# Optimization experiments

Hardware: AMD Instinct MI355X
Metric: run time of the kernel (lower is better)

Reference implementation:

```python
import jax, jax.numpy as jnp
import numpy as np

N, F, T, B, E, G = 50000, 3, 32, 32, 100000, 64
R = 1.1

def setup_inputs() -> dict:
    key = jax.random.key(0)
    k1, k2, k3, k4 = jax.random.split(key, 4)
    x = jax.random.normal(k1, (N, F), dtype=jnp.float32)
    v = jax.random.uniform(k2, (F, T), dtype=jnp.float32) - 0.5  # torch.rand(...) - 0.5
    lin = jnp.linspace(-R, R, B, dtype=jnp.float32).reshape(B, 1, 1)
    edge_index = jax.random.randint(k3, (2, E), 0, N)
    batch = jnp.sort(jax.random.randint(k4, (N,), 0, G))  # sorted graph ids per node
    return {"x": x, "v": v, "lin": lin, "edge_index": edge_index,
            "batch": batch, "num_graphs": G}


def _compute_ecc(h, index, lin, dim_size):
    # h: (M, T) heights; lin: (B,1,1); broadcast sigmoid -> (B, M, T)
    ecc = jax.nn.sigmoid(200.0 * (lin - h))
    # segment-sum over the M axis per graph; torch's segment_coo(...).movedim(0,1)
    # yields (dim_size, B, T), which equals segment_sum over axis 0 of (M, B, T).
    return jax.ops.segment_sum(jnp.moveaxis(ecc, 1, 0), index, num_segments=dim_size)


def reference(x, v, lin, edge_index, batch, num_graphs):
    nh = x @ v                                   # (N, T) node heights
    eh = jnp.max(nh[edge_index], axis=0)         # (E, T) edge max-gather
    ect_nodes = _compute_ecc(nh, batch, lin, num_graphs)                     # (G, B, T)
    ect_edges = _compute_ecc(eh, batch[edge_index[0]], lin, num_graphs)      # (G, B, T)
    return ect_nodes - ect_edges
```

## Files before the change

### kernel.cpp

```cpp
#include <hip/hip_runtime.h>

#define WG 256
#define G64 64
#define SPLITS 16

__global__ __launch_bounds__(WG) void k_bucket(const int* __restrict__ edge,
                                               const int* __restrict__ batch,
                                               int2* __restrict__ bucket,
                                               int* __restrict__ cursor,
                                               int* __restrict__ node_off,
                                               float* __restrict__ out,
                                               int E, int N, int CAP) {
    __shared__ int lc[G64], lb[G64];
    int tid = threadIdx.x;
    int bid = blockIdx.x;
    if (tid < G64) lc[tid] = 0;

    if (bid < G64) {
        float4* o4 = (float4*)(out + ((size_t)bid << 10));
        o4[tid] = make_float4(0.f, 0.f, 0.f, 0.f);
    }
    __syncthreads();

    int e = bid * WG + tid;
    int g = 0, r = 0, s = 0, d = 0;
    if (e < E) {
        s = edge[e];
        d = edge[E + e];
        g = batch[s];
        r = atomicAdd(&lc[g], 1);
    }
    __syncthreads();
    if (tid < G64 && lc[tid]) lb[tid] = atomicAdd(&cursor[tid], lc[tid]);
    __syncthreads();
    if (e < E) {
        int pos = lb[g] + r;
        if (pos < CAP) bucket[(size_t)g * CAP + pos] = make_int2(s, d);
    }

    if (bid == 0 && tid <= G64) {
        int lo = 0, hi = N;
        while (lo < hi) {
            int mid = (lo + hi) >> 1;
            if (batch[mid] < tid) lo = mid + 1; else hi = mid;
        }
        node_off[tid] = lo;
    }
}

__global__ __launch_bounds__(WG) void k_acc(const float* __restrict__ x,
                                            const float* __restrict__ v,
                                            const int2* __restrict__ bucket,
                                            const float* __restrict__ lin,
                                            const int* __restrict__ cursor,
                                            const int* __restrict__ node_off,
                                            float* __restrict__ out, int CAP) {
    int g = blockIdx.x;
    int n0 = node_off[g], n1 = node_off[g + 1];
    int nn = n1 - n0;
    int ne = cursor[g]; if (ne > CAP) ne = CAP;
    int L = nn + ne;
    int ipc = (L + SPLITS - 1) / SPLITS;
    int lo = blockIdx.y * ipc;
    int hi = lo + ipc; if (hi > L) hi = L;

    int tid = threadIdx.x, t = tid & 31, sub = tid >> 5;
    float v0 = v[t], v1 = v[32 + t], v2 = v[64 + t];

    float lin0 = lin[0];
    float dlin = lin[1] - lin[0];
    const float LOG2E = 1.4426950408889634f;
    float d2 = 200.f * dlin * LOG2E;
    float inv_dlin = 1.f / dlin;
    float fstep = exp2f(-d2);

    float acc[32];
#pragma unroll
    for (int b = 0; b < 32; ++b) acc[b] = 0.f;

    int nhi = hi < nn ? hi : nn;
    for (int idx = lo + sub; idx < nhi; idx += 8) {
        const float* xr = x + (size_t)(n0 + idx) * 3;
        float h = xr[0] * v0 + xr[1] * v1 + xr[2] * v2;
        float bs = (h - lin0) * inv_dlin;
        float bF = floorf(bs);
        float e0 = exp2f((bs - bF) * d2);
        float s0 = __builtin_amdgcn_rcpf(1.f + e0);
        float s1 = __builtin_amdgcn_rcpf(fmaf(e0, fstep, 1.f));
        float m = s1 - s0;
        float base = fmaf(-bF, m, s0);
#pragma unroll
        for (int b = 0; b < 32; ++b)
            acc[b] += __builtin_amdgcn_fmed3f(fmaf(m, (float)b, base), 0.f, 1.f);
    }

    int elo = lo > nn ? lo : nn;
    for (int idx = elo + sub; idx < hi; idx += 8) {
        int2 sd = bucket[(size_t)g * CAP + (idx - nn)];
        const float* xs = x + (size_t)sd.x * 3;
        const float* xd = x + (size_t)sd.y * 3;
        float hs = xs[0] * v0 + xs[1] * v1 + xs[2] * v2;
        float hd = xd[0] * v0 + xd[1] * v1 + xd[2] * v2;
        float h = fmaxf(hs, hd);
        float bs = (h - lin0) * inv_dlin;
        float bF = floorf(bs);
        float e0 = exp2f((bs - bF) * d2);
        float s0 = __builtin_amdgcn_rcpf(1.f + e0);
        float s1 = __builtin_amdgcn_rcpf(fmaf(e0, fstep, 1.f));
        float m = -(s1 - s0);
        float base = fmaf(-bF, m, -s0);
#pragma unroll
        for (int b = 0; b < 32; ++b)
            acc[b] += __builtin_amdgcn_fmed3f(fmaf(m, (float)b, base), -1.f, 0.f);
    }

    __shared__ float stage[4 * 1024];
#pragma unroll
    for (int b = 0; b < 32; ++b) acc[b] += __shfl_xor(acc[b], 32, 64);
    int w = tid >> 6;
    if ((tid & 32) == 0) {
#pragma unroll
        for (int b = 0; b < 32; ++b) stage[(w << 10) + (b << 5) + t] = acc[b];
    }
    __syncthreads();
    for (int c = tid; c < 1024; c += WG) {
        float s = stage[c] + stage[1024 + c] + stage[2048 + c] + stage[3072 + c];
        unsafeAtomicAdd(&out[((size_t)g << 10) + c], s);
    }
}

extern "C" void kernel_launch(void* const* d_in, const int* in_sizes, int n_in,
                              void* d_out, int out_size, void* d_ws, size_t ws_size,
                              hipStream_t stream) {
    const float* x     = (const float*)d_in[0];
    const float* v     = (const float*)d_in[1];
    const float* lin   = (const float*)d_in[2];
    const int*   edge  = (const int*)d_in[3];
    const int*   batch = (const int*)d_in[4];
    int N = in_sizes[4];
    int E = in_sizes[3] / 2;

    float* out = (float*)d_out;

    int* cursor   = (int*)d_ws;
    int* node_off = cursor + G64;
    int2* bucket  = (int2*)((char*)d_ws + 1024);
    long long cap_ws = (long long)((ws_size - 1024) / ((size_t)G64 * sizeof(int2)));
    int CAP = (int)(cap_ws < (long long)E ? cap_ws : (long long)E);

    hipMemsetAsync(cursor, 0, G64 * sizeof(int), stream);

    k_bucket<<<(E + WG - 1) / WG, WG, 0, stream>>>(edge, batch, bucket, cursor,
                                                   node_off, out, E, N, CAP);
    dim3 grid(G64, SPLITS);
    k_acc<<<grid, WG, 0, stream>>>(x, v, bucket, lin, cursor, node_off, out, CAP);
}
```

Baseline: 94.95 us.

## Fuse edge bucketing into accumulation kernel with per-block filtered edge scan

```diff
diff --git a/kernel.cpp b/kernel.cpp
--- a/kernel.cpp
+++ b/kernel.cpp
@@ -3,70 +3,49 @@
 #define WG 256
 #define G64 64
 #define SPLITS 16
+#define TILE 1024
 
-__global__ __launch_bounds__(WG) void k_bucket(const int* __restrict__ edge,
-                                               const int* __restrict__ batch,
-                                               int2* __restrict__ bucket,
-                                               int* __restrict__ cursor,
-                                               int* __restrict__ node_off,
-                                               float* __restrict__ out,
-                                               int E, int N, int CAP) {
-    __shared__ int lc[G64], lb[G64];
-    int tid = threadIdx.x;
-    int bid = blockIdx.x;
-    if (tid < G64) lc[tid] = 0;
 
-    if (bid < G64) {
-        float4* o4 = (float4*)(out + ((size_t)bid << 10));
-        o4[tid] = make_float4(0.f, 0.f, 0.f, 0.f);
-    }
+__device__ __forceinline__ int lbound_par(const int* __restrict__ batch, int N,
+                                          int val, int tid, int* scratch) {
+    const int stride = (N + WG - 1) / WG;
+    if (tid == 0) *scratch = N;
     __syncthreads();
-
-    int e = bid * WG + tid;
-    int g = 0, r = 0, s = 0, d = 0;
-    if (e < E) {
-        s = edge[e];
-        d = edge[E + e];
-        g = batch[s];
-        r = atomicAdd(&lc[g], 1);
-    }
+    int i0 = tid * stride;
+    if (i0 < N && batch[i0] >= val) atomicMin(scratch, i0);
     __syncthreads();
-    if (tid < G64 && lc[tid]) lb[tid] = atomicAdd(&cursor[tid], lc[tid]);
+    int hi = *scratch;
     __syncthreads();
-    if (e < E) {
-        int pos = lb[g] + r;
-        if (pos < CAP) bucket[(size_t)g * CAP + pos] = make_int2(s, d);
-    }
-
-    if (bid == 0 && tid <= G64) {
-        int lo = 0, hi = N;
-        while (lo < hi) {
-            int mid = (lo + hi) >> 1;
-            if (batch[mid] < tid) lo = mid + 1; else hi = mid;
-        }
-        node_off[tid] = lo;
-    }
+    if (tid == 0) *scratch = hi;
+    __syncthreads();
+    int lo = hi - stride + 1; if (lo < 0) lo = 0;
+    int j = lo + tid;
+    if (j < hi && batch[j] >= val) atomicMin(scratch, j);
+    __syncthreads();
+    int r = *scratch;
+    __syncthreads();
+    return r;
 }
 
-__global__ __launch_bounds__(WG) void k_acc(const float* __restrict__ x,
-                                            const float* __restrict__ v,
-                                            const int2* __restrict__ bucket,
-                                            const float* __restrict__ lin,
-                                            const int* __restrict__ cursor,
-                                            const int* __restrict__ node_off,
-                                            float* __restrict__ out, int CAP) {
-    int g = blockIdx.x;
-    int n0 = node_off[g], n1 = node_off[g + 1];
-    int nn = n1 - n0;
-    int ne = cursor[g]; if (ne > CAP) ne = CAP;
-    int L = nn + ne;
-    int ipc = (L + SPLITS - 1) / SPLITS;
-    int lo = blockIdx.y * ipc;
-    int hi = lo + ipc; if (hi > L) hi = L;
+__global__ __launch_bounds__(WG) void k_fused(const float* __restrict__ x,
+                                              const float* __restrict__ v,
+                                              const float* __restrict__ lin,
+                                              const int* __restrict__ edge,
+                                              const int* __restrict__ batch,
+                                              float* __restrict__ out,
+                                              int E, int N) {
+    __shared__ int2  queue[TILE];
+    __shared__ float stage[4 * 1024];
+    __shared__ int   qn, scratch;
 
+    int g = blockIdx.x, split = blockIdx.y;
     int tid = threadIdx.x, t = tid & 31, sub = tid >> 5;
+
+    int n0 = lbound_par(batch, N, g,     tid, &scratch);
+    int n1 = lbound_par(batch, N, g + 1, tid, &scratch);
+    if (tid == 0) qn = 0;
+
     float v0 = v[t], v1 = v[32 + t], v2 = v[64 + t];
-
     float lin0 = lin[0];
     float dlin = lin[1] - lin[0];
     const float LOG2E = 1.4426950408889634f;
@@ -78,9 +57,11 @@
 #pragma unroll
     for (int b = 0; b < 32; ++b) acc[b] = 0.f;
 
-    int nhi = hi < nn ? hi : nn;
-    for (int idx = lo + sub; idx < nhi; idx += 8) {
-        const float* xr = x + (size_t)(n0 + idx) * 3;
+    int nn = n1 - n0;
+    int a0 = n0 + (int)((long long)nn * split / SPLITS);
+    int a1 = n0 + (int)((long long)nn * (split + 1) / SPLITS);
+    for (int idx = a0 + sub; idx < a1; idx += 8) {
+        const float* xr = x + (size_t)idx * 3;
         float h = xr[0] * v0 + xr[1] * v1 + xr[2] * v2;
         float bs = (h - lin0) * inv_dlin;
         float bF = floorf(bs);
@@ -94,27 +75,43 @@
             acc[b] += __builtin_amdgcn_fmed3f(fmaf(m, (float)b, base), 0.f, 1.f);
     }
 
-    int elo = lo > nn ? lo : nn;
-    for (int idx = elo + sub; idx < hi; idx += 8) {
-        int2 sd = bucket[(size_t)g * CAP + (idx - nn)];
-        const float* xs = x + (size_t)sd.x * 3;
-        const float* xd = x + (size_t)sd.y * 3;
-        float hs = xs[0] * v0 + xs[1] * v1 + xs[2] * v2;
-        float hd = xd[0] * v0 + xd[1] * v1 + xd[2] * v2;
-        float h = fmaxf(hs, hd);
-        float bs = (h - lin0) * inv_dlin;
-        float bF = floorf(bs);
-        float e0 = exp2f((bs - bF) * d2);
-        float s0 = __builtin_amdgcn_rcpf(1.f + e0);
-        float s1 = __builtin_amdgcn_rcpf(fmaf(e0, fstep, 1.f));
-        float m = -(s1 - s0);
-        float base = fmaf(-bF, m, -s0);
+    int c0 = (int)((long long)E * split / SPLITS);
+    int c1 = (int)((long long)E * (split + 1) / SPLITS);
+    __syncthreads();
+    for (int ts = c0; ts < c1; ts += TILE) {
+        int te = ts + TILE; if (te > c1) te = c1;
+        for (int i = ts + tid; i < te; i += WG) {
+            int s = edge[i];
+            if (s >= n0 && s < n1) {
+                int k = atomicAdd(&qn, 1);
+                queue[k] = make_int2(s, edge[E + i]);
+            }
+        }
+        __syncthreads();
+        int q = qn;
+        for (int k = sub; k < q; k += 8) {
+            int2 sd = queue[k];
+            const float* xs = x + (size_t)sd.x * 3;
+            const float* xd = x + (size_t)sd.y * 3;
+            float hs = xs[0] * v0 + xs[1] * v1 + xs[2] * v2;
+            float hd = xd[0] * v0 + xd[1] * v1 + xd[2] * v2;
+            float h = fmaxf(hs, hd);
+            float bs = (h - lin0) * inv_dlin;
+            float bF = floorf(bs);
+            float e0 = exp2f((bs - bF) * d2);
+            float s0 = __builtin_amdgcn_rcpf(1.f + e0);
+            float s1 = __builtin_amdgcn_rcpf(fmaf(e0, fstep, 1.f));
+            float m = -(s1 - s0);
+            float base = fmaf(-bF, m, -s0);
 #pragma unroll
-        for (int b = 0; b < 32; ++b)
-            acc[b] += __builtin_amdgcn_fmed3f(fmaf(m, (float)b, base), -1.f, 0.f);
+            for (int b = 0; b < 32; ++b)
+                acc[b] += __builtin_amdgcn_fmed3f(fmaf(m, (float)b, base), -1.f, 0.f);
+        }
+        __syncthreads();
+        if (tid == 0) qn = 0;
+        __syncthreads();
     }
 
-    __shared__ float stage[4 * 1024];
 #pragma unroll
     for (int b = 0; b < 32; ++b) acc[b] += __shfl_xor(acc[b], 32, 64);
     int w = tid >> 6;
@@ -139,19 +136,11 @@
     const int*   batch = (const int*)d_in[4];
     int N = in_sizes[4];
     int E = in_sizes[3] / 2;
+    (void)d_ws; (void)ws_size; (void)n_in;
 
     float* out = (float*)d_out;
+    hipMemsetAsync(out, 0, (size_t)out_size * sizeof(float), stream);
 
-    int* cursor   = (int*)d_ws;
-    int* node_off = cursor + G64;
-    int2* bucket  = (int2*)((char*)d_ws + 1024);
-    long long cap_ws = (long long)((ws_size - 1024) / ((size_t)G64 * sizeof(int2)));
-    int CAP = (int)(cap_ws < (long long)E ? cap_ws : (long long)E);
-
-    hipMemsetAsync(cursor, 0, G64 * sizeof(int), stream);
-
-    k_bucket<<<(E + WG - 1) / WG, WG, 0, stream>>>(edge, batch, bucket, cursor,
-                                                   node_off, out, E, N, CAP);
     dim3 grid(G64, SPLITS);
-    k_acc<<<grid, WG, 0, stream>>>(x, v, bucket, lin, cursor, node_off, out, CAP);
+    k_fused<<<grid, WG, 0, stream>>>(x, v, lin, edge, batch, out, E, N);
 }
```

Result: slower. 105.5 us (+11.1%).
